# Kernel optimization log

Hardware: AMD Instinct MI355X
Metric: run time of the kernel (lower is better)

Reference implementation:

```python
import jax, jax.numpy as jnp
import numpy as np


def setup_inputs() -> dict:
    key = jax.random.key(0)
    ks = jax.random.split(key, 16)
    B, IMG, D_VQ, K, H, A = 65536, 32, 64, 512, 128, 128
    F = IMG * IMG  # 1024
    s = lambda fan_in: 1.0 / np.sqrt(fan_in)
    return {
        "x": jax.random.normal(ks[0], (B, IMG, IMG), jnp.float32),
        "W_e0": jax.random.normal(ks[1], (F, H), jnp.float32) * s(F),
        "b_e0": jnp.zeros((H,), jnp.float32),
        "W_e1": jax.random.normal(ks[2], (H, H), jnp.float32) * s(H),
        "b_e1": jnp.zeros((H,), jnp.float32),
        "W_e2": jax.random.normal(ks[3], (H, H), jnp.float32) * s(H),
        "b_e2": jnp.zeros((H,), jnp.float32),
        "W_p": jax.random.normal(ks[4], (F, D_VQ), jnp.float32) * s(F),
        "b_p": jnp.zeros((D_VQ,), jnp.float32),
        "E": jax.random.normal(ks[5], (K, D_VQ), jnp.float32) * s(D_VQ),
        "W_a0": jax.random.normal(ks[6], (H, H), jnp.float32) * s(H),
        "b_a0": jnp.zeros((H,), jnp.float32),
        "W_a1": jax.random.normal(ks[7], (H, A), jnp.float32) * s(H),
        "b_a1": jnp.zeros((A,), jnp.float32),
        "W_c0": jax.random.normal(ks[8], (H, H), jnp.float32) * s(H),
        "b_c0": jnp.zeros((H,), jnp.float32),
        "W_c1": jax.random.normal(ks[9], (H, H), jnp.float32) * s(H),
        "b_c1": jnp.zeros((H,), jnp.float32),
        "W_c2": jax.random.normal(ks[10], (H, 1), jnp.float32) * s(H),
        "b_c2": jnp.zeros((1,), jnp.float32),
    }


COMMITMENT_COST = 0.25


def reference(x, W_e0, b_e0, W_e1, b_e1, W_e2, b_e2, W_p, b_p, E,
              W_a0, b_a0, W_a1, b_a1, W_c0, b_c0, W_c1, b_c1, W_c2, b_c2):
    IMG = x.shape[-1]
    xf = x.reshape((-1, IMG * IMG))  # [B, 1024]

    # embedding MLP tower
    emb = jax.nn.relu(xf @ W_e0 + b_e0)
    emb = jax.nn.relu(emb @ W_e1 + b_e1)
    emb = jax.nn.relu(emb @ W_e2 + b_e2)

    # projection to VQ embedding dim (input width 1024 != 64)
    xq = xf @ W_p + b_p  # [B, 64]

    # Vector quantization: pairwise sq-distance via expansion, argmin, gather
    d = (jnp.sum(xq * xq, axis=1, keepdims=True)
         - 2.0 * (xq @ E.T)
         + jnp.sum(E * E, axis=1)[None, :])  # [B, K]
    idx = jnp.argmin(d, axis=1)  # [B]
    quantized = E[idx]           # one-hot @ E == gather, same math
    quantized = xq + jax.lax.stop_gradient(quantized - xq)
    e_latent = jnp.mean((jax.lax.stop_gradient(quantized) - xq) ** 2)
    q_latent = jnp.mean((quantized - jax.lax.stop_gradient(xq)) ** 2)
    vq_loss = q_latent + COMMITMENT_COST * e_latent

    # actor head
    a = jax.nn.relu(emb @ W_a0 + b_a0)
    probs = jax.nn.softmax(a @ W_a1 + b_a1)  # Categorical probs

    # critic head
    c = jax.nn.relu(emb @ W_c0 + b_c0)
    c = jax.nn.relu(c @ W_c1 + b_c1)
    critic = jnp.squeeze(c @ W_c2 + b_c2, axis=-1)  # [B]

    return probs, critic, vq_loss, idx
```

## Files before the change

kernel.cpp:

```cpp
#include <hip/hip_runtime.h>
#include <hip/hip_bf16.h>

#define F_IN   1024
#define H_DIM  128
#define D_VQE  64
#define K_CODES 512

typedef __attribute__((ext_vector_type(8))) short s8v;
typedef __attribute__((ext_vector_type(4))) float f4v;

static __device__ __forceinline__ unsigned f2bf(float f) {
    unsigned u = __builtin_bit_cast(unsigned, f);
    return (u + 0x7fffu + ((u >> 16) & 1u)) >> 16;
}

static __device__ __forceinline__ f4v mfma16x16x32(s8v a, s8v b, f4v c) {
    return __builtin_amdgcn_mfma_f32_16x16x32_bf16(a, b, c, 0, 0, 0);
}

__global__ __launch_bounds__(256) void conv_weights(
    const float* __restrict__ W0,
    const float* __restrict__ W1, const float* __restrict__ W2,
    const float* __restrict__ W3, const float* __restrict__ W4,
    const float* __restrict__ W5, const float* __restrict__ W6,
    short* __restrict__ out)
{
    int g = blockIdx.x * 256 + threadIdx.x;
    if (g < 131072) {
        int n = g >> 10, k = g & 1023;
        out[g] = (short)f2bf(W0[k * 128 + n]);
    } else {
        int r = g - 131072;
        int which = r >> 14, o = r & 16383;
        int n = o >> 7, k = o & 127;
        const float* Ws[6] = {W1, W2, W3, W4, W5, W6};
        out[131072 + which * 16384 + n * 128 + k] = (short)f2bf(Ws[which][k * 128 + n]);
    }
}

__global__ __launch_bounds__(256) void gemm_e0(
    const float* __restrict__ A,
    const short* __restrict__ Wt,
    const float* __restrict__ bias,
    short* __restrict__ out)
{
    __shared__ __align__(16) char smem[36864];
    short* As = (short*)smem;
    short* Bs = (short*)(smem + 18432);
    short* Cs = (short*)smem;

    const int t = threadIdx.x;
    const int lane = t & 63, w = t >> 6;
    const int l15 = lane & 15, q = lane >> 4;
    const size_t row0 = (size_t)blockIdx.x * 128;

    f4v acc[2][8];
#pragma unroll
    for (int i = 0; i < 2; ++i)
#pragma unroll
        for (int j = 0; j < 8; ++j) acc[i][j] = {0.f, 0.f, 0.f, 0.f};

    for (int ch = 0; ch < 16; ++ch) {
        __syncthreads();
#pragma unroll
        for (int i = 0; i < 8; ++i) {
            int c = t + 256 * i;
            int r = c >> 4, c4 = c & 15;
            float4 a4 = *(const float4*)(A + (row0 + r) * 1024 + ch * 64 + c4 * 4);
            unsigned p01 = f2bf(a4.x) | (f2bf(a4.y) << 16);
            unsigned p23 = f2bf(a4.z) | (f2bf(a4.w) << 16);
            *(int2*)(As + r * 72 + c4 * 4) = make_int2((int)p01, (int)p23);
        }
#pragma unroll
        for (int i = 0; i < 4; ++i) {
            int c = t + 256 * i;
            int n = c >> 3, c16 = c & 7;
            *(int4*)(Bs + n * 72 + c16 * 8) = *(const int4*)(Wt + (size_t)n * 1024 + ch * 64 + c16 * 8);
        }
        __syncthreads();
#pragma unroll
        for (int kc = 0; kc < 2; ++kc) {
            int kb = kc * 32 + q * 8;
            s8v a0 = *(const s8v*)(As + (w * 32 + l15) * 72 + kb);
            s8v a1 = *(const s8v*)(As + (w * 32 + 16 + l15) * 72 + kb);
#pragma unroll
            for (int ct = 0; ct < 8; ++ct) {
                s8v b = *(const s8v*)(Bs + (ct * 16 + l15) * 72 + kb);
                acc[0][ct] = mfma16x16x32(a0, b, acc[0][ct]);
                acc[1][ct] = mfma16x16x32(a1, b, acc[1][ct]);
            }
        }
    }

    float bias_v[8];
#pragma unroll
    for (int ct = 0; ct < 8; ++ct) bias_v[ct] = bias[ct * 16 + l15];

    __syncthreads();
#pragma unroll
    for (int rt = 0; rt < 2; ++rt)
#pragma unroll
        for (int ct = 0; ct < 8; ++ct)
#pragma unroll
            for (int reg = 0; reg < 4; ++reg) {
                float v = acc[rt][ct][reg] + bias_v[ct];
                v = fmaxf(v, 0.f);
                Cs[(w * 32 + rt * 16 + q * 4 + reg) * 136 + ct * 16 + l15] = (short)f2bf(v);
            }
    __syncthreads();
#pragma unroll
    for (int i = 0; i < 8; ++i) {
        int c = t + 256 * i;
        int r = c >> 4, c16 = c & 15;
        *(int4*)(out + (row0 + r) * 128 + c16 * 8) = *(const int4*)(Cs + r * 136 + c16 * 8);
    }
}

template<int MODE>
__global__ __launch_bounds__(256) void gemm_h(
    const short* __restrict__ A,
    const short* __restrict__ Wt,
    const float* __restrict__ bias,
    const float* __restrict__ w2,
    const float* __restrict__ b2,
    void* __restrict__ outv)
{
    __shared__ __align__(16) char smem[53248];
    short* As = (short*)smem;
    short* Bs = (short*)(smem + 18432);
    short* Cs = (short*)smem;

    const int t = threadIdx.x;
    const int lane = t & 63, w = t >> 6;
    const int l15 = lane & 15, q = lane >> 4;
    const size_t row0 = (size_t)blockIdx.x * 128;

#pragma unroll
    for (int i = 0; i < 8; ++i) {
        int c = t + 256 * i;
        int n = c >> 4, c16 = c & 15;
        *(int4*)(Bs + n * 136 + c16 * 8) = *(const int4*)(Wt + n * 128 + c16 * 8);
    }

    f4v acc[2][8];
#pragma unroll
    for (int i = 0; i < 2; ++i)
#pragma unroll
        for (int j = 0; j < 8; ++j) acc[i][j] = {0.f, 0.f, 0.f, 0.f};

#pragma unroll
    for (int half = 0; half < 2; ++half) {
        __syncthreads();
#pragma unroll
        for (int i = 0; i < 4; ++i) {
            int c = t + 256 * i;
            int r = c >> 3, c16 = c & 7;
            *(int4*)(As + r * 72 + c16 * 8) = *(const int4*)(A + (row0 + r) * 128 + half * 64 + c16 * 8);
        }
        __syncthreads();
#pragma unroll
        for (int kc = 0; kc < 2; ++kc) {
            int kb = kc * 32 + q * 8;
            int kg = half * 64 + kb;
            s8v a0 = *(const s8v*)(As + (w * 32 + l15) * 72 + kb);
            s8v a1 = *(const s8v*)(As + (w * 32 + 16 + l15) * 72 + kb);
#pragma unroll
            for (int ct = 0; ct < 8; ++ct) {
                s8v b = *(const s8v*)(Bs + (ct * 16 + l15) * 136 + kg);
                acc[0][ct] = mfma16x16x32(a0, b, acc[0][ct]);
                acc[1][ct] = mfma16x16x32(a1, b, acc[1][ct]);
            }
        }
    }

    float bias_v[8];
#pragma unroll
    for (int ct = 0; ct < 8; ++ct) bias_v[ct] = bias[ct * 16 + l15];

    if (MODE == 0) {
        short* out = (short*)outv;
        __syncthreads();
#pragma unroll
        for (int rt = 0; rt < 2; ++rt)
#pragma unroll
            for (int ct = 0; ct < 8; ++ct)
#pragma unroll
                for (int reg = 0; reg < 4; ++reg) {
                    float v = acc[rt][ct][reg] + bias_v[ct];
                    v = fmaxf(v, 0.f);
                    Cs[(w * 32 + rt * 16 + q * 4 + reg) * 136 + ct * 16 + l15] = (short)f2bf(v);
                }
        __syncthreads();
#pragma unroll
        for (int i = 0; i < 8; ++i) {
            int c = t + 256 * i;
            int r = c >> 4, c16 = c & 15;
            *(int4*)(out + (row0 + r) * 128 + c16 * 8) = *(const int4*)(Cs + r * 136 + c16 * 8);
        }
    } else if (MODE == 1) {
        float* out = (float*)outv;
#pragma unroll
        for (int rt = 0; rt < 2; ++rt)
#pragma unroll
            for (int reg = 0; reg < 4; ++reg) {
                size_t m = row0 + w * 32 + rt * 16 + q * 4 + reg;
                float v[8];
                float mx = -3.4e38f;
#pragma unroll
                for (int ct = 0; ct < 8; ++ct) { v[ct] = acc[rt][ct][reg] + bias_v[ct]; mx = fmaxf(mx, v[ct]); }
#pragma unroll
                for (int off = 1; off < 16; off <<= 1) mx = fmaxf(mx, __shfl_xor(mx, off, 64));
                float s = 0.f;
#pragma unroll
                for (int ct = 0; ct < 8; ++ct) { v[ct] = __expf(v[ct] - mx); s += v[ct]; }
#pragma unroll
                for (int off = 1; off < 16; off <<= 1) s += __shfl_xor(s, off, 64);
                float inv = 1.0f / s;
#pragma unroll
                for (int ct = 0; ct < 8; ++ct) out[m * 128 + ct * 16 + l15] = v[ct] * inv;
            }
    } else {
        float* out = (float*)outv;
        float w2v[8];
#pragma unroll
        for (int ct = 0; ct < 8; ++ct) w2v[ct] = w2[ct * 16 + l15];
        float b2s = b2[0];
#pragma unroll
        for (int rt = 0; rt < 2; ++rt)
#pragma unroll
            for (int reg = 0; reg < 4; ++reg) {
                size_t m = row0 + w * 32 + rt * 16 + q * 4 + reg;
                float p = 0.f;
#pragma unroll
                for (int ct = 0; ct < 8; ++ct) p += fmaxf(acc[rt][ct][reg] + bias_v[ct], 0.f) * w2v[ct];
#pragma unroll
                for (int off = 1; off < 16; off <<= 1) p += __shfl_xor(p, off, 64);
                if (l15 == 0) out[m] = p + b2s;
            }
    }
}

constexpr int BM = 64, BN = 64, BK = 16;

__global__ __launch_bounds__(256) void gemm_n64(
    const float* __restrict__ A, int lda,
    const float* __restrict__ W, int ldw,
    const float* __restrict__ bias,
    float* __restrict__ C, int ldc, int K)
{
    __shared__ float As[BK][BM + 4];
    __shared__ float Bs[BK][BN];
    const int t  = threadIdx.x;
    const int tx = t & 15, ty = t >> 4;
    const int row0 = blockIdx.x * BM;

    const int arow = t >> 2;
    const int ak   = (t & 3) << 2;
    const int bk   = t >> 4;
    const int bc   = (t & 15) << 2;

    const float* Ap = A + (size_t)(row0 + arow) * lda + ak;
    const float* Wp = W + (size_t)bk * ldw + bc;

    float acc[4][4] = {};
    for (int k0 = 0; k0 < K; k0 += BK) {
        float4 a4 = *(const float4*)(Ap + k0);
        float4 b4 = *(const float4*)(Wp + (size_t)k0 * ldw);
        As[ak + 0][arow] = a4.x;
        As[ak + 1][arow] = a4.y;
        As[ak + 2][arow] = a4.z;
        As[ak + 3][arow] = a4.w;
        *(float4*)&Bs[bk][bc] = b4;
        __syncthreads();
#pragma unroll
        for (int k = 0; k < BK; ++k) {
            float4 av = *(const float4*)&As[k][ty << 2];
            float4 bv = *(const float4*)&Bs[k][tx << 2];
            acc[0][0] += av.x * bv.x; acc[0][1] += av.x * bv.y; acc[0][2] += av.x * bv.z; acc[0][3] += av.x * bv.w;
            acc[1][0] += av.y * bv.x; acc[1][1] += av.y * bv.y; acc[1][2] += av.y * bv.z; acc[1][3] += av.y * bv.w;
            acc[2][0] += av.z * bv.x; acc[2][1] += av.z * bv.y; acc[2][2] += av.z * bv.z; acc[2][3] += av.z * bv.w;
            acc[3][0] += av.w * bv.x; acc[3][1] += av.w * bv.y; acc[3][2] += av.w * bv.z; acc[3][3] += av.w * bv.w;
        }
        __syncthreads();
    }

    float4 b4 = *(const float4*)(bias + (tx << 2));
#pragma unroll
    for (int i = 0; i < 4; ++i) {
        float4 o;
        o.x = acc[i][0] + b4.x; o.y = acc[i][1] + b4.y;
        o.z = acc[i][2] + b4.z; o.w = acc[i][3] + b4.w;
        *(float4*)(C + (size_t)(row0 + (ty << 2) + i) * ldc + (tx << 2)) = o;
    }
}

__global__ __launch_bounds__(256) void vq_kernel(
    const float* __restrict__ xq, const float* __restrict__ E,
    float* __restrict__ idx_out, float* __restrict__ accum)
{
    __shared__ float Es[128 * D_VQE];
    __shared__ float en[128];
    __shared__ float wsum[4];

    const int t = threadIdx.x;
    const size_t row = (size_t)blockIdx.x * 256 + t;

    float x[D_VQE];
    const float* xr = xq + row * D_VQE;
#pragma unroll
    for (int d = 0; d < D_VQE; d += 4) {
        float4 v = *(const float4*)(xr + d);
        x[d] = v.x; x[d + 1] = v.y; x[d + 2] = v.z; x[d + 3] = v.w;
    }
    float sx = 0.f;
#pragma unroll
    for (int d = 0; d < D_VQE; ++d) sx += x[d] * x[d];

    float best = 3.4e38f;
    int bj = 0;

    for (int q = 0; q < 4; ++q) {
        __syncthreads();
        const float4* src = (const float4*)(E + (size_t)q * 128 * D_VQE);
        float4* dst = (float4*)Es;
        for (int i = t; i < 128 * D_VQE / 4; i += 256) dst[i] = src[i];
        __syncthreads();
        if (t < 128) {
            float s = 0.f;
            const float* e = &Es[t * D_VQE];
#pragma unroll 8
            for (int d = 0; d < D_VQE; ++d) s += e[d] * e[d];
            en[t] = s;
        }
        __syncthreads();
        for (int j = 0; j < 128; ++j) {
            const float* e = &Es[j * D_VQE];
            float d0 = 0.f, d1 = 0.f, d2 = 0.f, d3 = 0.f;
#pragma unroll
            for (int d = 0; d < D_VQE; d += 4) {
                float4 ev = *(const float4*)(e + d);
                d0 += x[d]     * ev.x;
                d1 += x[d + 1] * ev.y;
                d2 += x[d + 2] * ev.z;
                d3 += x[d + 3] * ev.w;
            }
            float dot = (d0 + d1) + (d2 + d3);
            float dist = sx - 2.0f * dot + en[j];
            if (dist < best) { best = dist; bj = q * 128 + j; }
        }
    }

    idx_out[row] = (float)bj;

    float err = 0.f;
    const float* eb = E + (size_t)bj * D_VQE;
#pragma unroll
    for (int d = 0; d < D_VQE; d += 4) {
        float4 ev = *(const float4*)(eb + d);
        float e0 = ev.x - x[d], e1 = ev.y - x[d + 1], e2 = ev.z - x[d + 2], e3 = ev.w - x[d + 3];
        err += e0 * e0 + e1 * e1 + e2 * e2 + e3 * e3;
    }
    for (int off = 32; off > 0; off >>= 1) err += __shfl_down(err, off, 64);
    if ((t & 63) == 0) wsum[t >> 6] = err;
    __syncthreads();
    if (t == 0) atomicAdd(accum, wsum[0] + wsum[1] + wsum[2] + wsum[3]);
}

__global__ void vq_fin(const float* __restrict__ accum, float* __restrict__ out, float scale)
{
    out[0] = accum[0] * scale;
}

extern "C" void kernel_launch(void* const* d_in, const int* in_sizes, int n_in,
                              void* d_out, int out_size, void* d_ws, size_t ws_size,
                              hipStream_t stream)
{
    const float* x    = (const float*)d_in[0];
    const float* W_e0 = (const float*)d_in[1];
    const float* b_e0 = (const float*)d_in[2];
    const float* W_e1 = (const float*)d_in[3];
    const float* b_e1 = (const float*)d_in[4];
    const float* W_e2 = (const float*)d_in[5];
    const float* b_e2 = (const float*)d_in[6];
    const float* W_p  = (const float*)d_in[7];
    const float* b_p  = (const float*)d_in[8];
    const float* E    = (const float*)d_in[9];
    const float* W_a0 = (const float*)d_in[10];
    const float* b_a0 = (const float*)d_in[11];
    const float* W_a1 = (const float*)d_in[12];
    const float* b_a1 = (const float*)d_in[13];
    const float* W_c0 = (const float*)d_in[14];
    const float* b_c0 = (const float*)d_in[15];
    const float* W_c1 = (const float*)d_in[16];
    const float* b_c1 = (const float*)d_in[17];
    const float* W_c2 = (const float*)d_in[18];
    const float* b_c2 = (const float*)d_in[19];

    const size_t B = (size_t)in_sizes[0] / F_IN;

    short* buf0 = (short*)d_ws;
    short* buf1 = buf0 + B * H_DIM;
    short* wt   = buf1 + B * H_DIM;
    short* wt_e0 = wt;
    short* wt_e1 = wt + 131072;
    short* wt_e2 = wt_e1 + 16384;
    short* wt_a0 = wt_e2 + 16384;
    short* wt_a1 = wt_a0 + 16384;
    short* wt_c0 = wt_a1 + 16384;
    short* wt_c1 = wt_c0 + 16384;
    float* xq    = (float*)(wt + 229376);
    float* accum = xq + B * D_VQE;

    float* out   = (float*)d_out;
    float* probs = out;
    float* crit  = out + B * H_DIM;
    float* loss  = crit + B;
    float* idxo  = loss + 1;

    hipMemsetAsync(accum, 0, sizeof(float), stream);

    dim3 blk(256);
    const int nb64  = (int)(B / 64);
    const int nb128 = (int)(B / 128);

    conv_weights<<<dim3(896), blk, 0, stream>>>(W_e0, W_e1, W_e2, W_a0, W_a1, W_c0, W_c1, wt);

    gemm_n64<<<dim3(nb64), blk, 0, stream>>>(x, F_IN, W_p, D_VQE, b_p, xq, D_VQE, F_IN);
    vq_kernel<<<dim3((int)(B / 256)), blk, 0, stream>>>(xq, E, idxo, accum);
    vq_fin<<<1, 1, 0, stream>>>(accum, loss, 1.25f / ((float)B * (float)D_VQE));

    gemm_e0<<<dim3(nb128), blk, 0, stream>>>(x, wt_e0, b_e0, buf0);
    gemm_h<0><<<dim3(nb128), blk, 0, stream>>>(buf0, wt_e1, b_e1, nullptr, nullptr, buf1);
    gemm_h<0><<<dim3(nb128), blk, 0, stream>>>(buf1, wt_e2, b_e2, nullptr, nullptr, buf0);
    gemm_h<0><<<dim3(nb128), blk, 0, stream>>>(buf0, wt_a0, b_a0, nullptr, nullptr, buf1);
    gemm_h<1><<<dim3(nb128), blk, 0, stream>>>(buf1, wt_a1, b_a1, nullptr, nullptr, probs);
    gemm_h<0><<<dim3(nb128), blk, 0, stream>>>(buf0, wt_c0, b_c0, nullptr, nullptr, buf1);
    gemm_h<2><<<dim3(nb128), blk, 0, stream>>>(buf1, wt_c1, b_c1, W_c2, b_c2, crit);
}
```

Baseline: 782.3 us.

## Rewrite projection GEMM and split VQ argmin into register-resident partial and merge kernels

```diff
diff --git a/kernel.cpp b/kernel.cpp
--- a/kernel.cpp
+++ b/kernel.cpp
@@ -240,128 +240,140 @@
     }
 }
 
-constexpr int BM = 64, BN = 64, BK = 16;
-
-__global__ __launch_bounds__(256) void gemm_n64(
-    const float* __restrict__ A, int lda,
-    const float* __restrict__ W, int ldw,
+__global__ __launch_bounds__(256) void proj64(
+    const float* __restrict__ A,
+    const float* __restrict__ W,
     const float* __restrict__ bias,
-    float* __restrict__ C, int ldc, int K)
-{
-    __shared__ float As[BK][BM + 4];
-    __shared__ float Bs[BK][BN];
-    const int t  = threadIdx.x;
-    const int tx = t & 15, ty = t >> 4;
-    const int row0 = blockIdx.x * BM;
-
-    const int arow = t >> 2;
-    const int ak   = (t & 3) << 2;
-    const int bk   = t >> 4;
-    const int bc   = (t & 15) << 2;
-
-    const float* Ap = A + (size_t)(row0 + arow) * lda + ak;
-    const float* Wp = W + (size_t)bk * ldw + bc;
-
-    float acc[4][4] = {};
-    for (int k0 = 0; k0 < K; k0 += BK) {
-        float4 a4 = *(const float4*)(Ap + k0);
-        float4 b4 = *(const float4*)(Wp + (size_t)k0 * ldw);
-        As[ak + 0][arow] = a4.x;
-        As[ak + 1][arow] = a4.y;
-        As[ak + 2][arow] = a4.z;
-        As[ak + 3][arow] = a4.w;
-        *(float4*)&Bs[bk][bc] = b4;
-        __syncthreads();
-#pragma unroll
-        for (int k = 0; k < BK; ++k) {
-            float4 av = *(const float4*)&As[k][ty << 2];
-            float4 bv = *(const float4*)&Bs[k][tx << 2];
-            acc[0][0] += av.x * bv.x; acc[0][1] += av.x * bv.y; acc[0][2] += av.x * bv.z; acc[0][3] += av.x * bv.w;
-            acc[1][0] += av.y * bv.x; acc[1][1] += av.y * bv.y; acc[1][2] += av.y * bv.z; acc[1][3] += av.y * bv.w;
-            acc[2][0] += av.z * bv.x; acc[2][1] += av.z * bv.y; acc[2][2] += av.z * bv.z; acc[2][3] += av.z * bv.w;
-            acc[3][0] += av.w * bv.x; acc[3][1] += av.w * bv.y; acc[3][2] += av.w * bv.z; acc[3][3] += av.w * bv.w;
-        }
-        __syncthreads();
-    }
-
-    float4 b4 = *(const float4*)(bias + (tx << 2));
-#pragma unroll
-    for (int i = 0; i < 4; ++i) {
-        float4 o;
-        o.x = acc[i][0] + b4.x; o.y = acc[i][1] + b4.y;
-        o.z = acc[i][2] + b4.z; o.w = acc[i][3] + b4.w;
-        *(float4*)(C + (size_t)(row0 + (ty << 2) + i) * ldc + (tx << 2)) = o;
-    }
-}
-
-__global__ __launch_bounds__(256) void vq_kernel(
+    float* __restrict__ C)
+{
+    const int t = threadIdx.x;
+    const int lane = t & 63;
+    const int c0 = __builtin_amdgcn_readfirstlane((t >> 6) << 4);
+    const size_t row = (size_t)blockIdx.x * 64 + lane;
+    const float* xr = A + row * 1024;
+
+    float acc[16];
+#pragma unroll
+    for (int c = 0; c < 16; ++c) acc[c] = 0.f;
+
+    for (int k4 = 0; k4 < 1024; k4 += 4) {
+        float4 xv = *(const float4*)(xr + k4);
+        float xs[4] = {xv.x, xv.y, xv.z, xv.w};
+#pragma unroll
+        for (int kk = 0; kk < 4; ++kk) {
+            const float* wrow = W + (size_t)(k4 + kk) * 64 + c0;
+#pragma unroll
+            for (int c = 0; c < 16; ++c)
+                acc[c] = __builtin_fmaf(xs[kk], wrow[c], acc[c]);
+        }
+    }
+#pragma unroll
+    for (int c = 0; c < 16; c += 4) {
+        float4 o = {acc[c] + bias[c0 + c], acc[c + 1] + bias[c0 + c + 1],
+                    acc[c + 2] + bias[c0 + c + 2], acc[c + 3] + bias[c0 + c + 3]};
+        *(float4*)(C + row * 64 + c0 + c) = o;
+    }
+}
+
+__global__ __launch_bounds__(256) void vq_part(
     const float* __restrict__ xq, const float* __restrict__ E,
-    float* __restrict__ idx_out, float* __restrict__ accum)
-{
-    __shared__ float Es[128 * D_VQE];
-    __shared__ float en[128];
+    unsigned long long* __restrict__ part)
+{
+    __shared__ float sxs[64];
+    const int t = threadIdx.x;
+    const int lane = t & 63, w = t >> 6;
+    const size_t row0 = (size_t)blockIdx.x * 64;
+    const int j0 = 2 * t, j1 = 2 * t + 1;
+
+    float e0r[64], e1r[64];
+#pragma unroll
+    for (int d = 0; d < 64; d += 4) {
+        float4 v = *(const float4*)(E + (size_t)j0 * 64 + d);
+        e0r[d] = v.x; e0r[d + 1] = v.y; e0r[d + 2] = v.z; e0r[d + 3] = v.w;
+        float4 u = *(const float4*)(E + (size_t)j1 * 64 + d);
+        e1r[d] = u.x; e1r[d + 1] = u.y; e1r[d + 2] = u.z; e1r[d + 3] = u.w;
+    }
+    float en0 = 0.f, en1 = 0.f;
+#pragma unroll
+    for (int d = 0; d < 64; ++d) {
+        en0 = __builtin_fmaf(e0r[d], e0r[d], en0);
+        en1 = __builtin_fmaf(e1r[d], e1r[d], en1);
+    }
+
+    if (w == 0) {
+        const float* xr = xq + (row0 + lane) * 64;
+        float sx = 0.f;
+#pragma unroll
+        for (int d = 0; d < 64; d += 4) {
+            float4 v = *(const float4*)(xr + d);
+            sx = __builtin_fmaf(v.x, v.x, sx);
+            sx = __builtin_fmaf(v.y, v.y, sx);
+            sx = __builtin_fmaf(v.z, v.z, sx);
+            sx = __builtin_fmaf(v.w, v.w, sx);
+        }
+        sxs[lane] = sx;
+    }
+    __syncthreads();
+
+    for (int rr = 0; rr < 64; rr += 2) {
+        const float* x0 = xq + (row0 + rr) * 64;
+        const float* x1 = x0 + 64;
+        float a[2][2][4];
+#pragma unroll
+        for (int r = 0; r < 2; ++r)
+#pragma unroll
+            for (int cd = 0; cd < 2; ++cd)
+#pragma unroll
+                for (int c = 0; c < 4; ++c) a[r][cd][c] = 0.f;
+
+#pragma unroll
+        for (int d = 0; d < 64; ++d) {
+            float xv0 = x0[d];
+            float xv1 = x1[d];
+            int c = d & 3;
+            a[0][0][c] = __builtin_fmaf(xv0, e0r[d], a[0][0][c]);
+            a[0][1][c] = __builtin_fmaf(xv0, e1r[d], a[0][1][c]);
+            a[1][0][c] = __builtin_fmaf(xv1, e0r[d], a[1][0][c]);
+            a[1][1][c] = __builtin_fmaf(xv1, e1r[d], a[1][1][c]);
+        }
+
+#pragma unroll
+        for (int r = 0; r < 2; ++r) {
+            float sx = sxs[rr + r];
+            float dot0 = (a[r][0][0] + a[r][0][1]) + (a[r][0][2] + a[r][0][3]);
+            float dot1 = (a[r][1][0] + a[r][1][1]) + (a[r][1][2] + a[r][1][3]);
+            float dist0 = sx - 2.0f * dot0 + en0;
+            float dist1 = sx - 2.0f * dot1 + en1;
+            unsigned long long k0 = ((unsigned long long)__float_as_uint(dist0) << 32) | (unsigned)j0;
+            unsigned long long k1 = ((unsigned long long)__float_as_uint(dist1) << 32) | (unsigned)j1;
+            unsigned long long key = (k1 < k0) ? k1 : k0;
+#pragma unroll
+            for (int off = 1; off < 64; off <<= 1) {
+                unsigned long long o = __shfl_xor(key, off, 64);
+                if (o < key) key = o;
+            }
+            if (lane == 0) part[(row0 + rr + r) * 4 + w] = key;
+        }
+    }
+}
+
+__global__ __launch_bounds__(256) void vq_merge(
+    const unsigned long long* __restrict__ part,
+    float* __restrict__ idxo, float* __restrict__ accum)
+{
     __shared__ float wsum[4];
-
     const int t = threadIdx.x;
     const size_t row = (size_t)blockIdx.x * 256 + t;
-
-    float x[D_VQE];
-    const float* xr = xq + row * D_VQE;
-#pragma unroll
-    for (int d = 0; d < D_VQE; d += 4) {
-        float4 v = *(const float4*)(xr + d);
-        x[d] = v.x; x[d + 1] = v.y; x[d + 2] = v.z; x[d + 3] = v.w;
-    }
-    float sx = 0.f;
-#pragma unroll
-    for (int d = 0; d < D_VQE; ++d) sx += x[d] * x[d];
-
-    float best = 3.4e38f;
-    int bj = 0;
-
-    for (int q = 0; q < 4; ++q) {
-        __syncthreads();
-        const float4* src = (const float4*)(E + (size_t)q * 128 * D_VQE);
-        float4* dst = (float4*)Es;
-        for (int i = t; i < 128 * D_VQE / 4; i += 256) dst[i] = src[i];
-        __syncthreads();
-        if (t < 128) {
-            float s = 0.f;
-            const float* e = &Es[t * D_VQE];
-#pragma unroll 8
-            for (int d = 0; d < D_VQE; ++d) s += e[d] * e[d];
-            en[t] = s;
-        }
-        __syncthreads();
-        for (int j = 0; j < 128; ++j) {
-            const float* e = &Es[j * D_VQE];
-            float d0 = 0.f, d1 = 0.f, d2 = 0.f, d3 = 0.f;
-#pragma unroll
-            for (int d = 0; d < D_VQE; d += 4) {
-                float4 ev = *(const float4*)(e + d);
-                d0 += x[d]     * ev.x;
-                d1 += x[d + 1] * ev.y;
-                d2 += x[d + 2] * ev.z;
-                d3 += x[d + 3] * ev.w;
-            }
-            float dot = (d0 + d1) + (d2 + d3);
-            float dist = sx - 2.0f * dot + en[j];
-            if (dist < best) { best = dist; bj = q * 128 + j; }
-        }
-    }
-
-    idx_out[row] = (float)bj;
-
-    float err = 0.f;
-    const float* eb = E + (size_t)bj * D_VQE;
-#pragma unroll
-    for (int d = 0; d < D_VQE; d += 4) {
-        float4 ev = *(const float4*)(eb + d);
-        float e0 = ev.x - x[d], e1 = ev.y - x[d + 1], e2 = ev.z - x[d + 2], e3 = ev.w - x[d + 3];
-        err += e0 * e0 + e1 * e1 + e2 * e2 + e3 * e3;
-    }
-    for (int off = 32; off > 0; off >>= 1) err += __shfl_down(err, off, 64);
-    if ((t & 63) == 0) wsum[t >> 6] = err;
+    unsigned long long k = part[row * 4];
+#pragma unroll
+    for (int i = 1; i < 4; ++i) {
+        unsigned long long o = part[row * 4 + i];
+        if (o < k) k = o;
+    }
+    idxo[row] = (float)(unsigned)(k & 0xffffffffULL);
+    float dist = __uint_as_float((unsigned)(k >> 32));
+    for (int off = 32; off > 0; off >>= 1) dist += __shfl_down(dist, off, 64);
+    if ((t & 63) == 0) wsum[t >> 6] = dist;
     __syncthreads();
     if (t == 0) atomicAdd(accum, wsum[0] + wsum[1] + wsum[2] + wsum[3]);
 }
@@ -409,7 +421,8 @@
     short* wt_c0 = wt_a1 + 16384;
     short* wt_c1 = wt_c0 + 16384;
     float* xq    = (float*)(wt + 229376);
-    float* accum = xq + B * D_VQE;
+    unsigned long long* part = (unsigned long long*)(xq + B * D_VQE);
+    float* accum = (float*)(part + B * 4);
 
     float* out   = (float*)d_out;
     float* probs = out;
@@ -420,13 +433,13 @@
     hipMemsetAsync(accum, 0, sizeof(float), stream);
 
     dim3 blk(256);
-    const int nb64  = (int)(B / 64);
     const int nb128 = (int)(B / 128);
 
     conv_weights<<<dim3(896), blk, 0, stream>>>(W_e0, W_e1, W_e2, W_a0, W_a1, W_c0, W_c1, wt);
 
-    gemm_n64<<<dim3(nb64), blk, 0, stream>>>(x, F_IN, W_p, D_VQE, b_p, xq, D_VQE, F_IN);
-    vq_kernel<<<dim3((int)(B / 256)), blk, 0, stream>>>(xq, E, idxo, accum);
+    proj64<<<dim3((int)(B / 64)), blk, 0, stream>>>(x, W_p, b_p, xq);
+    vq_part<<<dim3((int)(B / 64)), blk, 0, stream>>>(xq, E, part);
+    vq_merge<<<dim3((int)(B / 256)), blk, 0, stream>>>(part, idxo, accum);
     vq_fin<<<1, 1, 0, stream>>>(accum, loss, 1.25f / ((float)B * (float)D_VQE));
 
     gemm_e0<<<dim3(nb128), blk, 0, stream>>>(x, wt_e0, b_e0, buf0);
```

New measurement: 741.7 us. -5.2%, faster.
